# Optimization experiments

Measured on AMD Instinct MI355X. Metric: run time of the kernel, lower is better.

The kernel has to match this reference:

```python
import jax, jax.numpy as jnp
import numpy as np

C = 1.0            # curvature args.c
EPS = 1e-7         # Hyperboloid eps for float32
MIN_NORM = 1e-15
MAX_SQDIST = 50.0
NUM_LAYERS = 3     # args.num_layers (resSumGCN hops)
MARGIN = 0.1       # args.margin
N_NODES = 200000
NUM_USERS = 100000
EMB_DIM = 64
E_ADJ = 1600000
E_TR = 65536
NUM_NEG = 16


def _mink_dot(x, y, keepdim=True):
    # Minkowski inner product: -x0*y0 + sum_i xi*yi
    res = jnp.sum(x * y, axis=-1) - 2.0 * x[..., 0] * y[..., 0]
    return res[..., None] if keepdim else res


def _sqdist(x, y, c):
    K = 1.0 / c
    prod = _mink_dot(x, y)                      # [E, 1]
    theta = jnp.maximum(-prod / K, 1.0 + EPS)
    return jnp.minimum(K * jnp.arccosh(theta) ** 2, MAX_SQDIST)


def _expmap0(u, c):
    sqrtK = (1.0 / c) ** 0.5
    x = u[..., 1:]
    x_norm = jnp.maximum(jnp.linalg.norm(x, axis=-1, keepdims=True), MIN_NORM)
    theta = x_norm / sqrtK
    first = sqrtK * jnp.cosh(theta)
    rest = sqrtK * jnp.sinh(theta) * x / x_norm
    return jnp.concatenate([first, rest], axis=-1)


def _logmap0(x, c):
    sqrtK = (1.0 / c) ** 0.5
    y = x[..., 1:]
    y_norm = jnp.maximum(jnp.linalg.norm(y, axis=-1, keepdims=True), MIN_NORM)
    theta = jnp.maximum(x[..., :1] / sqrtK, 1.0 + EPS)
    rest = sqrtK * jnp.arccosh(theta) * y / y_norm
    return jnp.concatenate([jnp.zeros_like(rest[..., :1]), rest], axis=-1)


def _proj(x, c):
    K = 1.0 / c
    y = x[..., 1:]
    first = jnp.sqrt(K + jnp.sum(y * y, axis=-1, keepdims=True))
    return jnp.concatenate([first, y], axis=-1)


def setup_inputs() -> dict:
    key = jax.random.key(0)
    ks = jax.random.split(key, 8)
    # embedding init: uniform(-scale, scale) tangent vector, then expmap0 onto hyperboloid
    tan = jax.random.uniform(ks[0], (N_NODES, EMB_DIM), minval=-0.1, maxval=0.1, dtype=jnp.float32)
    weight = _expmap0(tan, C)
    adj_row = jnp.sort(jax.random.randint(ks[1], (E_ADJ,), 0, N_NODES, dtype=jnp.int32))
    adj_col = jax.random.randint(ks[2], (E_ADJ,), 0, N_NODES, dtype=jnp.int32)
    # mimic symmetric-normalized adjacency values (~1/deg)
    adj_vals = jax.random.uniform(ks[3], (E_ADJ,), dtype=jnp.float32) * 0.125
    anchor = jax.random.randint(ks[4], (E_TR,), 0, NUM_USERS, dtype=jnp.int32)
    pos = jax.random.randint(ks[5], (E_TR,), 0, NUM_USERS, dtype=jnp.int32) + NUM_USERS
    neg = jax.random.randint(ks[6], (E_TR, NUM_NEG), 0, NUM_USERS, dtype=jnp.int32) + NUM_USERS
    return {"weight": weight, "adj_vals": adj_vals, "adj_row": adj_row,
            "adj_col": adj_col, "anchor": anchor, "pos": pos, "neg": neg}


def _encode(weight, adj_row, adj_col, adj_vals):
    # HypAgg: logmap0 -> resSumGCN (sum of adj^k x for k=1..L) -> expmap0 -> proj
    x_t = _logmap0(weight, C)
    h = x_t
    acc = jnp.zeros_like(x_t)
    for _ in range(NUM_LAYERS):
        h = jax.ops.segment_sum(adj_vals[:, None] * h[adj_col], adj_row,
                                num_segments=N_NODES, indices_are_sorted=True)
        acc = acc + h
    return _proj(_expmap0(acc, C), C)


def reference(weight, adj_vals, adj_row, adj_col, anchor, pos, neg):
    h = _encode(weight, adj_row, adj_col, adj_vals)      # [N, d] on hyperboloid
    emb_a = h[anchor]                                    # [E, d]
    emb_p = h[pos]                                       # [E, d]
    # decode_pos: sqdist + hratio weight
    pos_scores = _sqdist(emb_a, emb_p, C)                # [E, 1]
    u0 = emb_a[:, 0]
    i0 = emb_p[:, 0]
    score = (1.0 - _mink_dot(emb_a, emb_p, keepdim=False) - u0 - i0) / (u0 * i0)
    w = jax.nn.sigmoid(-score)[:, None]                  # [E, 1]
    # decode_neg: hard-negative mining (euclidean sqdist to positive, take min)
    d2 = jnp.sum((h[neg] - emb_p[:, None, :]) ** 2, axis=-1)   # [E, num_neg]
    hard_idx = jnp.argmin(d2, axis=1)
    hard_neg = jnp.take_along_axis(neg, hard_idx[:, None], axis=1)[:, 0]
    neg_scores = _sqdist(emb_a, h[hard_neg], C)          # [E, 1]
    # margin ranking loss with hyperbolic-ratio weight
    loss = jnp.sum(jnp.maximum(pos_scores - neg_scores + MARGIN * w, 0.0))
    return loss
```

## Files before the change

### kernel.cpp

```cpp
#include <hip/hip_runtime.h>
#include <hip/hip_bf16.h>
#include <math.h>

#define N_NODES 200000
#define EMB_DIM 64
#define E_ADJ 1600000
#define E_TR 65536
#define NUM_NEG 16
#define EPS 1e-7f
#define MIN_NORM 1e-15f
#define MAX_SQDIST 50.0f
#define MARGIN 0.1f
#define LOSS_BLOCKS (E_TR / 4)
#define SPMM_BLOCKS 2048
#define NWAVES (SPMM_BLOCKS * 4)

#define PACK_BLOCKS ((E_ADJ + 255) / 256)
#define RP_BLOCKS   ((N_NODES + 1 + 255) / 256)
#define LOG_BLOCKS  ((N_NODES + 15) / 16)

typedef float f4 __attribute__((ext_vector_type(4)));

__device__ __forceinline__ float group_reduce16(float v) {
    v += __shfl_xor(v, 8, 64);
    v += __shfl_xor(v, 4, 64);
    v += __shfl_xor(v, 2, 64);
    v += __shfl_xor(v, 1, 64);
    return v;
}

__device__ __forceinline__ float dot4(f4 a, f4 b) {
    return a.x * b.x + a.y * b.y + a.z * b.z + a.w * b.w;
}

__device__ __forceinline__ unsigned bfr(float f) {
    unsigned u = __float_as_uint(f);
    return (u + 0x7fffu + ((u >> 16) & 1u)) >> 16;
}
__device__ __forceinline__ uint2 f42bf(f4 v) {
    return make_uint2(bfr(v.x) | (bfr(v.y) << 16), bfr(v.z) | (bfr(v.w) << 16));
}
__device__ __forceinline__ f4 bf2f4(uint2 g) {
    f4 r;
    r.x = __uint_as_float(g.x << 16);
    r.y = __uint_as_float(g.x & 0xffff0000u);
    r.z = __uint_as_float(g.y << 16);
    r.w = __uint_as_float(g.y & 0xffff0000u);
    return r;
}

__global__ void prelude_kernel(const int* __restrict__ cols, const float* __restrict__ vals,
                               int2* __restrict__ ev, const int* __restrict__ rows,
                               int* __restrict__ rp, const float* __restrict__ w,
                               uint2* __restrict__ xt) {
    int b = blockIdx.x;
    if (b < PACK_BLOCKS) {
        int i = b * 256 + threadIdx.x;
        if (i < E_ADJ) ev[i] = make_int2(cols[i] << 4, __float_as_int(vals[i]));
    } else if (b < PACK_BLOCKS + RP_BLOCKS) {
        int r = (b - PACK_BLOCKS) * 256 + threadIdx.x;
        if (r <= N_NODES) {
            int lo = 0, hi = E_ADJ;
            while (lo < hi) {
                int mid = (lo + hi) >> 1;
                if (rows[mid] < r) lo = mid + 1; else hi = mid;
            }
            rp[r] = lo;
        }
    } else {
        int bb = b - PACK_BLOCKS - RP_BLOCKS;
        int wave = bb * 4 + (threadIdx.x >> 6);
        int lane = threadIdx.x & 63;
        int e = lane >> 4, d = lane & 15;
        int node = wave * 4 + e;
        if (node < N_NODES) {
            f4 v = ((const f4*)w)[(node << 4) + d];
            f4 y = v;
            if (d == 0) y.x = 0.0f;
            float n2 = group_reduce16(dot4(y, y));
            float ynorm = fmaxf(sqrtf(n2), MIN_NORM);
            float w0 = __shfl(v.x, lane & 48, 64);
            float theta = fmaxf(w0, 1.0f + EPS);
            float scale = acoshf(theta) / ynorm;
            xt[(node << 4) + d] = f42bf(y * scale);
        }
    }
}

__device__ __forceinline__ f4 spmm_row(const uint2* __restrict__ h_in,
                                       const int2* __restrict__ ev,
                                       int s, int eend, int e, int d) {
    f4 acc = {0.f, 0.f, 0.f, 0.f};
    int i = s;
    for (; i + 8 <= eend; i += 8) {
        int2 cv0 = ev[i + e];
        int2 cv1 = ev[i + 4 + e];
        uint2 g0 = h_in[cv0.x + d];
        uint2 g1 = h_in[cv1.x + d];
        acc += bf2f4(g0) * __int_as_float(cv0.y);
        acc += bf2f4(g1) * __int_as_float(cv1.y);
    }
    if (i + 4 <= eend) {
        int2 cv = ev[i + e];
        uint2 g = h_in[cv.x + d];
        acc += bf2f4(g) * __int_as_float(cv.y);
        i += 4;
    }
    if (i + e < eend) {
        int2 cv = ev[i + e];
        uint2 g = h_in[cv.x + d];
        acc += bf2f4(g) * __int_as_float(cv.y);
    }
    acc.x += __shfl_xor(acc.x, 16, 64); acc.y += __shfl_xor(acc.y, 16, 64);
    acc.z += __shfl_xor(acc.z, 16, 64); acc.w += __shfl_xor(acc.w, 16, 64);
    acc.x += __shfl_xor(acc.x, 32, 64); acc.y += __shfl_xor(acc.y, 32, 64);
    acc.z += __shfl_xor(acc.z, 32, 64); acc.w += __shfl_xor(acc.w, 32, 64);
    return acc;
}

__global__ void spmm_kernel(const uint2* __restrict__ h_in, uint2* __restrict__ h_out,
                            const int2* __restrict__ ev, const int* __restrict__ rp) {
    int lane = threadIdx.x & 63;
    int e = lane >> 4, d = lane & 15;
    int wid = __builtin_amdgcn_readfirstlane(blockIdx.x * 4 + (threadIdx.x >> 6));
    int row = wid;
    if (row >= N_NODES) return;
    int s = rp[row], eend = rp[row + 1];
    for (;;) {
        int nrow = row + NWAVES;
        int ns = 0, nend = 0;
        if (nrow < N_NODES) { ns = rp[nrow]; nend = rp[nrow + 1]; }
        f4 acc = spmm_row(h_in, ev, s, eend, e, d);
        if (e == 0)
            h_out[(row << 4) + d] = f42bf(acc);
        if (nrow >= N_NODES) break;
        row = nrow; s = ns; eend = nend;
    }
}

__global__ void spmm_expmap_kernel(const uint2* __restrict__ h_gather,
                                   const uint2* __restrict__ h1, const uint2* __restrict__ h2,
                                   float* __restrict__ h, float* __restrict__ nrm2,
                                   const int2* __restrict__ ev, const int* __restrict__ rp) {
    int lane = threadIdx.x & 63;
    int e = lane >> 4, d = lane & 15;
    int wid = __builtin_amdgcn_readfirstlane(blockIdx.x * 4 + (threadIdx.x >> 6));
    int row = wid;
    if (row >= N_NODES) return;
    int s = rp[row], eend = rp[row + 1];
    for (;;) {
        int nrow = row + NWAVES;
        int ns = 0, nend = 0;
        if (nrow < N_NODES) { ns = rp[nrow]; nend = rp[nrow + 1]; }
        int oi = (row << 4) + d;
        f4 a1 = bf2f4(h1[oi]);
        f4 a2 = bf2f4(h2[oi]);
        f4 acc = spmm_row(h_gather, ev, s, eend, e, d);
        f4 u = (a1 + a2) + acc;
        f4 x = u;
        if (d == 0) x.x = 0.0f;
        float n2 = group_reduce16(dot4(x, x));
        float xn = fmaxf(sqrtf(n2), MIN_NORM);
        float sh = sinhf(xn);
        f4 rest = x * (sh / xn);
        float r2 = group_reduce16(dot4(rest, rest));
        float first = sqrtf(1.0f + r2);
        f4 ov = rest;
        if (d == 0) ov.x = first;
        if (e == 0) {
            ((f4*)h)[oi] = ov;
            if (d == 0) nrm2[row] = first * first + r2;
        }
        if (nrow >= N_NODES) break;
        row = nrow; s = ns; eend = nend;
    }
}

__global__ void loss_kernel(const float* __restrict__ h, const float* __restrict__ nrm2,
                            const int* __restrict__ anchor, const int* __restrict__ pos,
                            const int* __restrict__ neg, float* __restrict__ partials) {
    int wib = threadIdx.x >> 6;
    int lane = threadIdx.x & 63;
    int e = lane >> 4, d = lane & 15;
    int i = __builtin_amdgcn_readfirstlane(blockIdx.x * 4 + wib);
    const f4* H = (const f4*)h;

    int ia = anchor[i], ip = pos[i];
    f4 a4 = H[(ia << 4) + d];
    f4 p4 = H[(ip << 4) + d];
    int4 nb4 = ((const int4*)(neg + (size_t)i * NUM_NEG))[e];

    float s[4];
    s[0] = dot4(p4, H[(nb4.x << 4) + d]);
    s[1] = dot4(p4, H[(nb4.y << 4) + d]);
    s[2] = dot4(p4, H[(nb4.z << 4) + d]);
    s[3] = dot4(p4, H[(nb4.w << 4) + d]);
    float dap = dot4(a4, p4);

    {
        bool hi = (d & 8) != 0;
        float send0 = hi ? s[0] : s[2];
        float send1 = hi ? s[1] : s[3];
        float r0 = __shfl_xor(send0, 8, 64);
        float r1 = __shfl_xor(send1, 8, 64);
        float k0 = hi ? s[2] : s[0];
        float k1 = hi ? s[3] : s[1];
        s[0] = k0 + r0;
        s[1] = k1 + r1;
    }
    float sv;
    {
        bool hi = (d & 4) != 0;
        float send = hi ? s[0] : s[1];
        float r = __shfl_xor(send, 4, 64);
        float k = hi ? s[1] : s[0];
        sv = k + r;
    }
    sv += __shfl_xor(sv, 2, 64);
    sv += __shfl_xor(sv, 1, 64);
    int b_lane = ((d >> 3) & 1) * 2 + ((d >> 2) & 1);
    int nidx_lane = (d & 8) ? ((d & 4) ? nb4.w : nb4.z)
                            : ((d & 4) ? nb4.y : nb4.x);
    int j_lane = 4 * e + b_lane;

    float np2 = nrm2[ip];
    float bd = nrm2[nidx_lane] + np2 - 2.0f * sv;
    int bj = j_lane;
    #pragma unroll
    for (int off = 32; off > 0; off >>= 1) {
        float od = __shfl_xor(bd, off, 64);
        int   oj = __shfl_xor(bj, off, 64);
        if (od < bd || (od == bd && oj < bj)) { bd = od; bj = oj; }
    }
    int bn = neg[(size_t)i * NUM_NEG + __builtin_amdgcn_readfirstlane(bj)];
    f4 w4 = H[(bn << 4) + d];
    float dan = group_reduce16(dot4(a4, w4));
    dap = group_reduce16(dap);

    float loss = 0.0f;
    if (lane == 0) {
        float a0 = a4.x, p0 = p4.x, n0 = w4.x;
        float mink = dap - 2.0f * a0 * p0;
        float th = fmaxf(-mink, 1.0f + EPS);
        float ac = acoshf(th);
        float pos_score = fminf(ac * ac, MAX_SQDIST);
        float score = (1.0f - mink - a0 - p0) / (a0 * p0);
        float wgt = 1.0f / (1.0f + expf(score));
        float minkn = dan - 2.0f * a0 * n0;
        float thn = fmaxf(-minkn, 1.0f + EPS);
        float acn = acoshf(thn);
        float neg_score = fminf(acn * acn, MAX_SQDIST);
        loss = fmaxf(pos_score - neg_score + MARGIN * wgt, 0.0f);
    }
    __shared__ float part[4];
    if (lane == 0) part[wib] = loss;
    __syncthreads();
    if (threadIdx.x == 0)
        partials[blockIdx.x] = part[0] + part[1] + part[2] + part[3];
}

__global__ void reduce_kernel(const float* __restrict__ partials, float* __restrict__ out) {
    int tid = threadIdx.x;
    float s = 0.0f;
    for (int i = tid; i < LOSS_BLOCKS; i += 1024)
        s += partials[i];
    #pragma unroll
    for (int off = 32; off > 0; off >>= 1)
        s += __shfl_xor(s, off, 64);
    __shared__ float part[16];
    if ((tid & 63) == 0) part[tid >> 6] = s;
    __syncthreads();
    if (tid == 0) {
        float t = 0.0f;
        #pragma unroll
        for (int k = 0; k < 16; ++k) t += part[k];
        out[0] = t;
    }
}

extern "C" void kernel_launch(void* const* d_in, const int* in_sizes, int n_in,
                              void* d_out, int out_size, void* d_ws, size_t ws_size,
                              hipStream_t stream) {
    const float* weight   = (const float*)d_in[0];
    const float* adj_vals = (const float*)d_in[1];
    const int*   adj_row  = (const int*)d_in[2];
    const int*   adj_col  = (const int*)d_in[3];
    const int*   anchor   = (const int*)d_in[4];
    const int*   pos      = (const int*)d_in[5];
    const int*   neg      = (const int*)d_in[6];
    float* out = (float*)d_out;

    const size_t NODEF32 = (size_t)N_NODES * EMB_DIM * sizeof(float);
    const size_t NODEBF  = (size_t)N_NODES * EMB_DIM * sizeof(unsigned short);
    const size_t MB = 1024 * 1024;
    char* ws = (char*)d_ws;
    float* hfin = (float*)(ws);
    uint2* bf0  = (uint2*)(ws + NODEF32);
    uint2* bf1  = (uint2*)(ws + NODEF32 + NODEBF);
    uint2* bf2  = (uint2*)(ws + NODEF32 + 2 * NODEBF);
    int*   rp   = (int*)  (ws + NODEF32 + 3 * NODEBF);
    float* nrm2 = (float*)(ws + NODEF32 + 3 * NODEBF + 1 * MB);
    int2*  ev   = (int2*) (ws + NODEF32 + 3 * NODEBF + 2 * MB);
    float* partials = (float*)(ws + NODEF32 + 3 * NODEBF + 16 * MB);

    prelude_kernel<<<PACK_BLOCKS + RP_BLOCKS + LOG_BLOCKS, 256, 0, stream>>>(
        adj_col, adj_vals, ev, adj_row, rp, weight, bf0);
    spmm_kernel<<<SPMM_BLOCKS, 256, 0, stream>>>(bf0, bf1, ev, rp);
    spmm_kernel<<<SPMM_BLOCKS, 256, 0, stream>>>(bf1, bf2, ev, rp);
    spmm_expmap_kernel<<<SPMM_BLOCKS, 256, 0, stream>>>(bf2, bf1, bf2, hfin, nrm2, ev, rp);
    loss_kernel<<<LOSS_BLOCKS, 256, 0, stream>>>(hfin, nrm2, anchor, pos, neg, partials);
    reduce_kernel<<<1, 1024, 0, stream>>>(partials, out);
}
```

Measured before the change: 361.2 us.

## Assign contiguous row blocks per wave and stage edge lists in LDS

Both SpMM kernels now give each wave a contiguous run of 25 rows instead of rows strided across the grid. Each wave copies its rows' packed (col, val) edge entries into a per-wave LDS buffer, then reads them from LDS in the row loop, falling back to global memory once past the 512-entry cap. The aim is better locality for the row-pointer and edge reads, with the edge-list fetch done in one coalesced burst. The cost is an extra LDS copy, a block-wide barrier, and more LDS per block, while the random feature gathers that likely dominate are unchanged.

```diff
diff --git a/kernel.cpp b/kernel.cpp
--- a/kernel.cpp
+++ b/kernel.cpp
@@ -14,6 +14,8 @@
 #define LOSS_BLOCKS (E_TR / 4)
 #define SPMM_BLOCKS 2048
 #define NWAVES (SPMM_BLOCKS * 4)
+#define RPW 25
+#define LDS_CAP 512
 
 #define PACK_BLOCKS ((E_ADJ + 255) / 256)
 #define RP_BLOCKS   ((N_NODES + 1 + 255) / 256)
@@ -87,27 +89,38 @@
     }
 }
 
-__device__ __forceinline__ f4 spmm_row(const uint2* __restrict__ h_in,
-                                       const int2* __restrict__ ev,
-                                       int s, int eend, int e, int d) {
+__device__ __forceinline__ f4 spmm_row_lds(const uint2* __restrict__ h_in,
+                                           const int2* __restrict__ ev,
+                                           const int2* L, int ebase, int staged,
+                                           int s, int re, int e, int d) {
     f4 acc = {0.f, 0.f, 0.f, 0.f};
     int i = s;
-    for (; i + 8 <= eend; i += 8) {
-        int2 cv0 = ev[i + e];
-        int2 cv1 = ev[i + 4 + e];
+    for (; i + 8 <= re; i += 8) {
+        int2 cv0, cv1;
+        if (i + 8 - ebase <= staged) {
+            cv0 = L[i - ebase + e];
+            cv1 = L[i - ebase + 4 + e];
+        } else {
+            cv0 = ev[i + e];
+            cv1 = ev[i + 4 + e];
+        }
         uint2 g0 = h_in[cv0.x + d];
         uint2 g1 = h_in[cv1.x + d];
         acc += bf2f4(g0) * __int_as_float(cv0.y);
         acc += bf2f4(g1) * __int_as_float(cv1.y);
     }
-    if (i + 4 <= eend) {
-        int2 cv = ev[i + e];
+    if (i + 4 <= re) {
+        int2 cv;
+        if (i + 4 - ebase <= staged) cv = L[i - ebase + e];
+        else                         cv = ev[i + e];
         uint2 g = h_in[cv.x + d];
         acc += bf2f4(g) * __int_as_float(cv.y);
         i += 4;
     }
-    if (i + e < eend) {
-        int2 cv = ev[i + e];
+    if (i + e < re) {
+        int2 cv;
+        if (re - ebase <= staged) cv = L[i - ebase + e];
+        else                      cv = ev[i + e];
         uint2 g = h_in[cv.x + d];
         acc += bf2f4(g) * __int_as_float(cv.y);
     }
@@ -118,44 +131,68 @@
     return acc;
 }
 
-__global__ void spmm_kernel(const uint2* __restrict__ h_in, uint2* __restrict__ h_out,
-                            const int2* __restrict__ ev, const int* __restrict__ rp) {
+__global__ __launch_bounds__(256) void spmm_kernel(const uint2* __restrict__ h_in,
+                                                   uint2* __restrict__ h_out,
+                                                   const int2* __restrict__ ev,
+                                                   const int* __restrict__ rp) {
+    __shared__ int2 evs[4][LDS_CAP];
+    int wib = threadIdx.x >> 6;
     int lane = threadIdx.x & 63;
     int e = lane >> 4, d = lane & 15;
-    int wid = __builtin_amdgcn_readfirstlane(blockIdx.x * 4 + (threadIdx.x >> 6));
-    int row = wid;
-    if (row >= N_NODES) return;
-    int s = rp[row], eend = rp[row + 1];
-    for (;;) {
-        int nrow = row + NWAVES;
-        int ns = 0, nend = 0;
-        if (nrow < N_NODES) { ns = rp[nrow]; nend = rp[nrow + 1]; }
-        f4 acc = spmm_row(h_in, ev, s, eend, e, d);
+    int wid = __builtin_amdgcn_readfirstlane(blockIdx.x * 4 + wib);
+    int r0 = wid * RPW;
+    if (r0 >= N_NODES) return;
+    int r1 = min(r0 + RPW, N_NODES);
+    int ebase = rp[r0];
+    int etot  = rp[r1];
+    int staged = min(etot - ebase, LDS_CAP);
+    int2* L = evs[wib];
+    for (int k = lane; k < staged; k += 64)
+        L[k] = ev[ebase + k];
+    __syncthreads();
+
+    int s = ebase;
+    int re = rp[r0 + 1];
+    for (int row = r0; row < r1; ++row) {
+        int re_next = (row + 1 < r1) ? rp[row + 2] : 0;
+        f4 acc = spmm_row_lds(h_in, ev, L, ebase, staged, s, re, e, d);
         if (e == 0)
             h_out[(row << 4) + d] = f42bf(acc);
-        if (nrow >= N_NODES) break;
-        row = nrow; s = ns; eend = nend;
-    }
-}
-
-__global__ void spmm_expmap_kernel(const uint2* __restrict__ h_gather,
-                                   const uint2* __restrict__ h1, const uint2* __restrict__ h2,
-                                   float* __restrict__ h, float* __restrict__ nrm2,
-                                   const int2* __restrict__ ev, const int* __restrict__ rp) {
+        s = re; re = re_next;
+    }
+}
+
+__global__ __launch_bounds__(256) void spmm_expmap_kernel(const uint2* __restrict__ h_gather,
+                                                          const uint2* __restrict__ h1,
+                                                          const uint2* __restrict__ h2,
+                                                          float* __restrict__ h,
+                                                          float* __restrict__ nrm2,
+                                                          const int2* __restrict__ ev,
+                                                          const int* __restrict__ rp) {
+    __shared__ int2 evs[4][LDS_CAP];
+    int wib = threadIdx.x >> 6;
     int lane = threadIdx.x & 63;
     int e = lane >> 4, d = lane & 15;
-    int wid = __builtin_amdgcn_readfirstlane(blockIdx.x * 4 + (threadIdx.x >> 6));
-    int row = wid;
-    if (row >= N_NODES) return;
-    int s = rp[row], eend = rp[row + 1];
-    for (;;) {
-        int nrow = row + NWAVES;
-        int ns = 0, nend = 0;
-        if (nrow < N_NODES) { ns = rp[nrow]; nend = rp[nrow + 1]; }
+    int wid = __builtin_amdgcn_readfirstlane(blockIdx.x * 4 + wib);
+    int r0 = wid * RPW;
+    if (r0 >= N_NODES) return;
+    int r1 = min(r0 + RPW, N_NODES);
+    int ebase = rp[r0];
+    int etot  = rp[r1];
+    int staged = min(etot - ebase, LDS_CAP);
+    int2* L = evs[wib];
+    for (int k = lane; k < staged; k += 64)
+        L[k] = ev[ebase + k];
+    __syncthreads();
+
+    int s = ebase;
+    int re = rp[r0 + 1];
+    for (int row = r0; row < r1; ++row) {
+        int re_next = (row + 1 < r1) ? rp[row + 2] : 0;
         int oi = (row << 4) + d;
         f4 a1 = bf2f4(h1[oi]);
         f4 a2 = bf2f4(h2[oi]);
-        f4 acc = spmm_row(h_gather, ev, s, eend, e, d);
+        f4 acc = spmm_row_lds(h_gather, ev, L, ebase, staged, s, re, e, d);
         f4 u = (a1 + a2) + acc;
         f4 x = u;
         if (d == 0) x.x = 0.0f;
@@ -171,8 +208,7 @@
             ((f4*)h)[oi] = ov;
             if (d == 0) nrm2[row] = first * first + r2;
         }
-        if (nrow >= N_NODES) break;
-        row = nrow; s = ns; eend = nend;
+        s = re; re = re_next;
     }
 }
 
```

Result: faster. 353.2 us (-2.2%).
